# Kernel optimization log

Hardware: AMD Instinct MI355X
Metric: run time of the kernel (lower is better)

The kernel has to match this reference:

```python
import jax, jax.numpy as jnp
import numpy as np

DIM = 768
NUM_HEADS = 12
MAX_DIST = 32


def _build_relative_index(max_dist):
    # Faithful port of the torch buffer construction (pure numpy, static).
    ii, jj = np.meshgrid(np.arange(max_dist), np.arange(max_dist), indexing='ij')
    coords_flat = np.stack([ii.reshape(-1), jj.reshape(-1)], axis=0)  # [2, max_dist^2]
    rel = coords_flat[:, :, None] - coords_flat[:, None, :]          # [2, L, L]
    rel = rel.transpose(1, 2, 0) + (max_dist - 1)
    rel_index = rel[:, :, 0] * (2 * max_dist - 1) + rel[:, :, 1]
    return jnp.asarray(rel_index, dtype=jnp.int32)                   # [L, L]


def setup_inputs() -> dict:
    key = jax.random.key(0)
    k_x, k_qkv, k_proj, k_pb, k_bt = jax.random.split(key, 5)
    B, N, C = 8, 1024, DIM
    std = 0.02
    x = jax.random.normal(k_x, (B, N, C), dtype=jnp.float32)
    qkv_w = jax.random.normal(k_qkv, (C, 3 * C), dtype=jnp.float32) * std  # Linear(dim, 3*dim, bias=False)
    proj_w = jax.random.normal(k_proj, (C, C), dtype=jnp.float32) * std
    proj_b = jax.random.normal(k_pb, (C,), dtype=jnp.float32) * std
    bias_table = jax.random.normal(k_bt, ((2 * MAX_DIST - 1) ** 2, NUM_HEADS), dtype=jnp.float32) * std
    rel_index = _build_relative_index(MAX_DIST)
    return {"x": x, "qkv_w": qkv_w, "proj_w": proj_w, "proj_b": proj_b,
            "bias_table": bias_table, "rel_index": rel_index}


def reference(x, qkv_w, proj_w, proj_b, bias_table, rel_index):
    B, N, C = x.shape
    H = NUM_HEADS
    hd = C // H
    scale = hd ** -0.5
    qkv = (x @ qkv_w).reshape(B, N, 3, H, hd)
    q, k, v = qkv[:, :, 0], qkv[:, :, 1], qkv[:, :, 2]          # [B, N, H, hd]
    attn = jnp.einsum('bnhd,bmhd->bhnm', q, k) * scale           # [B, H, N, N]
    # gathered relative position bias, added per head before softmax
    rel_bias = bias_table[rel_index[:N, :N].reshape(-1)]         # [N*N, H]
    rel_bias = rel_bias.reshape(N, N, H).transpose(2, 0, 1)      # [H, N, N]
    attn = jax.nn.softmax(attn + rel_bias[None], axis=-1)
    out = jnp.einsum('bhnm,bmhd->bnhd', attn, v).reshape(B, N, C)
    return out @ proj_w + proj_b
```

## Files before the change

kernel.cpp:

```cpp
#include <hip/hip_runtime.h>
#include <hip/hip_bf16.h>
#include <stdint.h>

typedef unsigned short u16;
typedef __attribute__((ext_vector_type(8))) short short8;
typedef __attribute__((ext_vector_type(4))) short short4v;
typedef __attribute__((ext_vector_type(8))) __bf16 bf16x8;
typedef __attribute__((ext_vector_type(4))) float floatx4;

typedef const uint32_t __attribute__((address_space(1))) *gptr1;
typedef uint32_t __attribute__((address_space(3))) *lptr3;

#define DIMC 768
#define NH   12
#define HD   64
#define NB   8
#define SEQ  1024
#define MROWS (NB*SEQ)
#define BTAB_N 47628
#define PB_N   768
#define LOG2E 1.44269504088896340736f

__device__ __forceinline__ float bf2f(u16 u){ return __uint_as_float(((uint32_t)u)<<16); }
__device__ __forceinline__ u16 f2bf(float f){
  uint32_t u = __float_as_uint(f);
  u += 0x7fffu + ((u>>16)&1u);
  return (u16)(u>>16);
}
__device__ __forceinline__ uint32_t pkbf(float lo, float hi){
  return (uint32_t)f2bf(lo) | ((uint32_t)f2bf(hi) << 16);
}
__device__ __forceinline__ floatx4 mfma16(short8 a, short8 b, floatx4 c){
  return __builtin_amdgcn_mfma_f32_16x16x32_bf16(
      __builtin_bit_cast(bf16x8, a), __builtin_bit_cast(bf16x8, b), c, 0, 0, 0);
}
__device__ __forceinline__ floatx4 mfma1k(short4v a, short4v b, floatx4 c){
  return __builtin_amdgcn_mfma_f32_16x16x16bf16_1k(a, b, c, 0, 0, 0);
}

__global__ __launch_bounds__(256) void detect_dtype(
    const u16* __restrict__ x, int* __restrict__ flag)
{
  __shared__ int cnt[256];
  int c = 0;
  for (int i = threadIdx.x; i < 2048; i += 256) {
    int e = (x[i] >> 7) & 0xFF;
    c += (e >= 0x8E);
  }
  cnt[threadIdx.x] = c;
  __syncthreads();
  for (int s = 128; s > 0; s >>= 1) {
    if ((int)threadIdx.x < s) cnt[threadIdx.x] += cnt[threadIdx.x + s];
    __syncthreads();
  }
  if (threadIdx.x == 0) *flag = (cnt[0] > 16) ? 1 : 0;
}

__global__ __launch_bounds__(256) void convert_x(
    const void* __restrict__ in, u16* __restrict__ outp,
    const int* __restrict__ flag, int n4)
{
  int idx = blockIdx.x * 256 + threadIdx.x;
  if (idx >= n4) return;
  ushort4 o;
  if (*flag) {
    const float4 v = ((const float4*)in)[idx];
    o.x = f2bf(v.x); o.y = f2bf(v.y); o.z = f2bf(v.z); o.w = f2bf(v.w);
  } else {
    o = ((const ushort4*)in)[idx];
  }
  ((ushort4*)outp)[idx] = o;
}

__global__ __launch_bounds__(256) void convert_small(
    const void* __restrict__ btab, const void* __restrict__ pb,
    u16* __restrict__ btabB, u16* __restrict__ pbB, const int* __restrict__ flag)
{
  int f = *flag;
  int idx = blockIdx.x * 256 + threadIdx.x;
  if (idx < BTAB_N) {
    float v = f ? ((const float*)btab)[idx] : bf2f(((const u16*)btab)[idx]);
    btabB[idx] = f2bf(v * LOG2E);
  } else if (idx < BTAB_N + PB_N) {
    int j = idx - BTAB_N;
    pbB[j] = f ? f2bf(((const float*)pb)[j]) : ((const u16*)pb)[j];
  }
}

__global__ __launch_bounds__(256) void transpose_any(
    const void* __restrict__ in, u16* __restrict__ out, int R, int C,
    const int* __restrict__ flag)
{
  __shared__ __align__(16) u16 t[64][65];
  const int f = *flag;
  const size_t bo = (size_t)blockIdx.z * R * C;
  const int r0 = blockIdx.y * 64, c0 = blockIdx.x * 64;
  const int tx = threadIdx.x & 63, ty = threadIdx.x >> 6;
  #pragma unroll
  for (int i = ty; i < 64; i += 4) {
    size_t src = bo + (size_t)(r0 + i) * C + c0 + tx;
    t[i][tx] = f ? f2bf(((const float*)in)[src]) : ((const u16*)in)[src];
  }
  __syncthreads();
  #pragma unroll
  for (int i = ty; i < 64; i += 4)
    out[bo + (size_t)(c0 + i) * R + r0 + tx] = t[tx][i];
}

__global__ __launch_bounds__(256) void build_bias(
    const int* __restrict__ rel, const u16* __restrict__ table, u16* __restrict__ biasM)
{
  const int t = blockIdx.x * 256 + threadIdx.x;
  const int idx = rel[t];
  const u16* row = table + idx * NH;
  #pragma unroll
  for (int h = 0; h < NH; ++h)
    biasM[(size_t)h * (SEQ * SEQ) + t] = row[h];
}

__global__ __launch_bounds__(256) void gemm_qkv(
    const u16* __restrict__ A, const u16* __restrict__ Bt,
    u16* __restrict__ Qb, u16* __restrict__ Kb, u16* __restrict__ Vt)
{
  const int K = DIMC;
  __shared__ __align__(16) u16 As[128 * 64];
  __shared__ __align__(16) u16 Bs[128 * 64];
  const int m0 = blockIdx.x * 128, n0 = blockIdx.y * 128;
  const int tid = threadIdx.x;
  const int wave = tid >> 6, lane = tid & 63;
  const int wx = wave & 1, wy = wave >> 1;
  const int r15 = lane & 15, quad = lane >> 4;
  const int sw = r15 & 7;

  const floatx4 zf = {0.f, 0.f, 0.f, 0.f};
  floatx4 acc[4][4];
  #pragma unroll
  for (int i = 0; i < 4; ++i)
    #pragma unroll
    for (int j = 0; j < 4; ++j) acc[i][j] = zf;

  for (int kt = 0; kt < K; kt += 64) {
    __syncthreads();
    #pragma unroll
    for (int s = 0; s < 4; ++s) {
      int c = s * 256 + wave * 64 + lane;
      int row = c >> 3, cc = (c & 7) ^ (row & 7);
      __builtin_amdgcn_global_load_lds(
          (gptr1)(const void*)&A[(size_t)(m0 + row) * K + kt + cc * 8],
          (lptr3)(void*)&As[c * 8], 16, 0, 0);
      __builtin_amdgcn_global_load_lds(
          (gptr1)(const void*)&Bt[(size_t)(n0 + row) * K + kt + cc * 8],
          (lptr3)(void*)&Bs[c * 8], 16, 0, 0);
    }
    __syncthreads();
    #pragma unroll
    for (int ks = 0; ks < 64; ks += 32) {
      const int kc = ks >> 3;
      short8 a[4], b[4];
      #pragma unroll
      for (int i = 0; i < 4; ++i)
        a[i] = *(const short8*)&As[(wy * 64 + i * 16 + r15) * 64 + ((kc + quad) ^ sw) * 8];
      #pragma unroll
      for (int j = 0; j < 4; ++j)
        b[j] = *(const short8*)&Bs[(wx * 64 + j * 16 + r15) * 64 + ((kc + quad) ^ sw) * 8];
      #pragma unroll
      for (int i = 0; i < 4; ++i)
        #pragma unroll
        for (int j = 0; j < 4; ++j)
          acc[i][j] = mfma16(a[i], b[j], acc[i][j]);
    }
  }

  #pragma unroll
  for (int i = 0; i < 4; ++i)
    #pragma unroll
    for (int j = 0; j < 4; ++j)
      #pragma unroll
      for (int g = 0; g < 4; ++g) {
        int gm = m0 + wy * 64 + i * 16 + quad * 4 + g;
        int gn = n0 + wx * 64 + j * 16 + r15;
        float v = acc[i][j][g];
        int three = gn / DIMC;
        int hn = gn - three * DIMC;
        int h = hn >> 6, d = hn & 63;
        int b_ = gm >> 10, n = gm & 1023;
        int bh = b_ * NH + h;
        if (three == 0)      Qb[(((size_t)bh) * SEQ + n) * HD + d] = f2bf(v * (0.125f * LOG2E));
        else if (three == 1) Kb[(((size_t)bh) * SEQ + n) * HD + d] = f2bf(v);
        else                 Vt[(((size_t)bh) * HD + d) * SEQ + n] = f2bf(v);
      }
}

__global__ __launch_bounds__(256) void gemm_proj(
    const u16* __restrict__ A, const u16* __restrict__ Bt,
    float* __restrict__ Out, const u16* __restrict__ bias)
{
  const int K = DIMC, N = DIMC;
  __shared__ __align__(16) u16 As[64 * 64];
  __shared__ __align__(16) u16 Bs[128 * 64];
  const int m0 = blockIdx.x * 64, n0 = blockIdx.y * 128;
  const int tid = threadIdx.x;
  const int wave = tid >> 6, lane = tid & 63;
  const int wy = wave >> 1, wx = wave & 1;
  const int r15 = lane & 15, quad = lane >> 4;
  const int sw = r15 & 7;

  const floatx4 zf = {0.f, 0.f, 0.f, 0.f};
  floatx4 acc[2][4];
  #pragma unroll
  for (int i = 0; i < 2; ++i)
    #pragma unroll
    for (int j = 0; j < 4; ++j) acc[i][j] = zf;

  for (int kt = 0; kt < K; kt += 64) {
    __syncthreads();
    #pragma unroll
    for (int s = 0; s < 2; ++s) {
      int c = tid + s * 256;
      int row = c >> 3, cc = (c & 7) ^ (row & 7);
      __builtin_amdgcn_global_load_lds(
          (gptr1)(const void*)&A[(size_t)(m0 + row) * K + kt + cc * 8],
          (lptr3)(void*)&As[c * 8], 16, 0, 0);
    }
    #pragma unroll
    for (int s = 0; s < 4; ++s) {
      int c = tid + s * 256;
      int row = c >> 3, cc = (c & 7) ^ (row & 7);
      __builtin_amdgcn_global_load_lds(
          (gptr1)(const void*)&Bt[(size_t)(n0 + row) * K + kt + cc * 8],
          (lptr3)(void*)&Bs[c * 8], 16, 0, 0);
    }
    __syncthreads();
    #pragma unroll
    for (int ks = 0; ks < 64; ks += 32) {
      const int kc = ks >> 3;
      short8 a[2], b[4];
      #pragma unroll
      for (int i = 0; i < 2; ++i)
        a[i] = *(const short8*)&As[(wy * 32 + i * 16 + r15) * 64 + ((kc + quad) ^ sw) * 8];
      #pragma unroll
      for (int j = 0; j < 4; ++j)
        b[j] = *(const short8*)&Bs[(wx * 64 + j * 16 + r15) * 64 + ((kc + quad) ^ sw) * 8];
      #pragma unroll
      for (int i = 0; i < 2; ++i)
        #pragma unroll
        for (int j = 0; j < 4; ++j)
          acc[i][j] = mfma16(a[i], b[j], acc[i][j]);
    }
  }

  #pragma unroll
  for (int i = 0; i < 2; ++i)
    #pragma unroll
    for (int j = 0; j < 4; ++j)
      #pragma unroll
      for (int g = 0; g < 4; ++g) {
        int gm = m0 + wy * 32 + i * 16 + quad * 4 + g;
        int gn = n0 + wx * 64 + j * 16 + r15;
        Out[(size_t)gm * N + gn] = acc[i][j][g] + bf2f(bias[gn]);
      }
}

template<int USEB>
__global__ __launch_bounds__(512, 6) void attention(
    const u16* __restrict__ Qb, const u16* __restrict__ Kb, const u16* __restrict__ Vt,
    const u16* __restrict__ biasB, u16* __restrict__ Ob)
{
  __shared__ __align__(16) u16 Qs[128 * 64];
  __shared__ __align__(16) u16 Ks[64 * 64];
  __shared__ __align__(16) u16 Vs[64 * 64];

  const int bh = blockIdx.x;
  const int h = bh % NH, b_ = bh / NH;
  const int q0 = blockIdx.y * 128;
  const int tid = threadIdx.x;
  const int wave = tid >> 6, lane = tid & 63;
  const int r15 = lane & 15, quad = lane >> 4;
  const int sw = r15 & 7;

  const u16* Qp = Qb + (size_t)bh * SEQ * HD;
  const u16* Kp = Kb + (size_t)bh * SEQ * HD;
  const u16* Vp = Vt + (size_t)bh * HD * SEQ;
  const u16* Bp = USEB ? (biasB + (size_t)h * SEQ * SEQ) : biasB;

  #pragma unroll
  for (int s = 0; s < 2; ++s) {
    int c = tid + s * 512;
    int row = c >> 3, cc = (c & 7) ^ (row & 7);
    __builtin_amdgcn_global_load_lds(
        (gptr1)(const void*)&Qp[(size_t)(q0 + row) * HD + cc * 8],
        (lptr3)(void*)&Qs[c * 8], 16, 0, 0);
  }

  const int q = q0 + wave * 16 + r15;
  const size_t bqoff = (size_t)q * SEQ;
  const int qrow = wave * 16 + r15;

  const floatx4 zf = {0.f, 0.f, 0.f, 0.f};
  floatx4 o[4];
  #pragma unroll
  for (int Jm = 0; Jm < 4; ++Jm) o[Jm] = zf;
  float lpart = 0.f;

  for (int kt = 0; kt < 16; ++kt) {
    __syncthreads();
    ushort4 bc[4];
    if (USEB) {
      #pragma unroll
      for (int Jk = 0; Jk < 4; ++Jk)
        bc[Jk] = *(const ushort4*)&Bp[bqoff + kt * 64 + Jk * 16 + quad * 4];
    }
    {
      int c = tid;
      int row = c >> 3, cc = (c & 7) ^ (row & 7);
      __builtin_amdgcn_global_load_lds(
          (gptr1)(const void*)&Kp[(size_t)(kt * 64 + row) * HD + cc * 8],
          (lptr3)(void*)&Ks[c * 8], 16, 0, 0);
      __builtin_amdgcn_global_load_lds(
          (gptr1)(const void*)&Vp[(size_t)row * SEQ + kt * 64 + cc * 8],
          (lptr3)(void*)&Vs[c * 8], 16, 0, 0);
    }
    __syncthreads();

    floatx4 sT[4];
    #pragma unroll
    for (int Jk = 0; Jk < 4; ++Jk) sT[Jk] = zf;

    #pragma unroll
    for (int ks = 0; ks < 64; ks += 32) {
      const int kc = ks >> 3;
      const short8 bq = *(const short8*)&Qs[qrow * 64 + ((kc + quad) ^ sw) * 8];
      #pragma unroll
      for (int Jk = 0; Jk < 4; ++Jk) {
        const short8 ak = *(const short8*)&Ks[(Jk * 16 + r15) * 64 + ((kc + quad) ^ sw) * 8];
        sT[Jk] = mfma16(ak, bq, sT[Jk]);
      }
    }

    #pragma unroll
    for (int Jk = 0; Jk < 4; ++Jk) {
      if (USEB) {
        sT[Jk][0] += bf2f(bc[Jk].x); sT[Jk][1] += bf2f(bc[Jk].y);
        sT[Jk][2] += bf2f(bc[Jk].z); sT[Jk][3] += bf2f(bc[Jk].w);
      } else {
        #pragma unroll
        for (int g = 0; g < 4; ++g) {
          const int k = kt * 64 + Jk * 16 + quad * 4 + g;
          const int idx = ((q >> 5) - (k >> 5) + 31) * 63 + ((q & 31) - (k & 31) + 31);
          sT[Jk][g] += bf2f(Bp[idx * NH + h]);
        }
      }
      const float p0 = exp2f(sT[Jk][0]);
      const float p1 = exp2f(sT[Jk][1]);
      const float p2v = exp2f(sT[Jk][2]);
      const float p3 = exp2f(sT[Jk][3]);
      lpart += (p0 + p1) + (p2v + p3);
      uint2 pw;
      pw.x = pkbf(p0, p1);
      pw.y = pkbf(p2v, p3);
      const short4v bp = __builtin_bit_cast(short4v, pw);
      const int vcol = ((2 * Jk + (quad >> 1)) ^ sw) * 8 + (quad & 1) * 4;
      #pragma unroll
      for (int Jm = 0; Jm < 4; ++Jm) {
        const short4v av = *(const short4v*)&Vs[(Jm * 16 + r15) * 64 + vcol];
        o[Jm] = mfma1k(av, bp, o[Jm]);
      }
    }
  }

  float l = lpart;
  l += __shfl_xor(l, 16, 64);
  l += __shfl_xor(l, 32, 64);
  const float inv = 1.0f / l;

  #pragma unroll
  for (int Jm = 0; Jm < 4; ++Jm) {
    uint2 st;
    st.x = pkbf(o[Jm][0] * inv, o[Jm][1] * inv);
    st.y = pkbf(o[Jm][2] * inv, o[Jm][3] * inv);
    *(uint2*)&Ob[((size_t)(b_ * SEQ + q)) * DIMC + h * HD + Jm * 16 + quad * 4] = st;
  }
}

extern "C" void kernel_launch(void* const* d_in, const int* in_sizes, int n_in,
                              void* d_out, int out_size, void* d_ws, size_t ws_size,
                              hipStream_t stream)
{
  (void)in_sizes; (void)n_in; (void)out_size;
  const void* x_raw  = d_in[0];
  const void* qkv_w  = d_in[1];
  const void* proj_w = d_in[2];
  const void* proj_b = d_in[3];
  const void* btab   = d_in[4];
  const int*  rel    = (const int*)d_in[5];
  float* out = (float*)d_out;

  const size_t SZ_FLAG = 256;
  const size_t SZ_XB   = (size_t)MROWS * DIMC * 2;
  const size_t SZ_BTAB = (BTAB_N * 2 + 255) & ~(size_t)255;
  const size_t SZ_PB   = (PB_N * 2 + 255) & ~(size_t)255;
  const size_t SZ_WQT  = (size_t)3 * DIMC * DIMC * 2;
  const size_t SZ_WPT  = (size_t)DIMC * DIMC * 2;
  const size_t SZ_T    = (size_t)NB * NH * SEQ * HD * 2;
  const size_t SZ_BM   = (size_t)NH * SEQ * SEQ * 2;
  const size_t NEED_FULL = SZ_FLAG + SZ_XB + SZ_BTAB + SZ_PB + SZ_WQT + SZ_WPT
                         + 3 * SZ_T + SZ_BM;

  char* p = (char*)d_ws;
  int* flag  = (int*)p;  p += SZ_FLAG;
  u16* xB    = (u16*)p;  p += SZ_XB;
  u16* btabB = (u16*)p;  p += SZ_BTAB;
  u16* pbB   = (u16*)p;  p += SZ_PB;
  u16* wqT   = (u16*)p;  p += SZ_WQT;
  u16* wpT   = (u16*)p;  p += SZ_WPT;
  u16* Qb    = (u16*)p;  p += SZ_T;
  u16* Kb    = (u16*)p;  p += SZ_T;
  u16* Vt    = (u16*)p;  p += SZ_T;
  u16* biasM = (u16*)p;

  const bool useBiasM = (ws_size >= NEED_FULL);
  const int n4 = MROWS * DIMC / 4;

  detect_dtype<<<1, 256, 0, stream>>>((const u16*)x_raw, flag);
  convert_x<<<(n4 + 255) / 256, 256, 0, stream>>>(x_raw, xB, flag, n4);
  convert_small<<<(BTAB_N + PB_N + 255) / 256, 256, 0, stream>>>(btab, proj_b, btabB, pbB, flag);
  transpose_any<<<dim3(3 * DIMC / 64, DIMC / 64, 1), 256, 0, stream>>>(qkv_w, wqT, DIMC, 3 * DIMC, flag);
  transpose_any<<<dim3(DIMC / 64, DIMC / 64, 1), 256, 0, stream>>>(proj_w, wpT, DIMC, DIMC, flag);
  gemm_qkv<<<dim3(MROWS / 128, 3 * DIMC / 128), 256, 0, stream>>>(
      xB, wqT, Qb, Kb, Vt);
  if (useBiasM) {
    build_bias<<<SEQ * SEQ / 256, 256, 0, stream>>>(rel, btabB, biasM);
    attention<1><<<dim3(NB * NH, SEQ / 128), 512, 0, stream>>>(Qb, Kb, Vt, biasM, xB);
  } else {
    attention<0><<<dim3(NB * NH, SEQ / 128), 512, 0, stream>>>(Qb, Kb, Vt, btabB, xB);
  }
  gemm_proj<<<dim3(MROWS / 64, DIMC / 128), 256, 0, stream>>>(
      xB, wpT, out, pbB);
}
```

Baseline: 268.9 us.

## Fuse all preprocessing kernels into one prep launch and enlarge proj GEMM tile

Replaces the dtype detection, x conversion, small-table conversion, two weight transposes and bias-matrix build with a single multi-job prep kernel. Each block recomputes the dtype flag locally through a wave reduction, so the separate flag kernel and its global round trip disappear. The bias matrix is now built straight from the raw table rather than from the converted copy. The output projection GEMM moves from 64x128 to 128x128 tiles, which gives more MFMA reuse per block but launches fewer blocks and needs more registers per thread.

```diff
diff --git a/kernel.cpp b/kernel.cpp
--- a/kernel.cpp
+++ b/kernel.cpp
@@ -21,6 +21,12 @@
 #define PB_N   768
 #define LOG2E 1.44269504088896340736f
 
+#define PJ_X     6144
+#define PJ_WQ    (PJ_X + 432)
+#define PJ_WP    (PJ_WQ + 144)
+#define PJ_BIAS  (PJ_WP + 4096)
+#define PJ_SMALL (PJ_BIAS + 190)
+
 __device__ __forceinline__ float bf2f(u16 u){ return __uint_as_float(((uint32_t)u)<<16); }
 __device__ __forceinline__ u16 f2bf(float f){
   uint32_t u = __float_as_uint(f);
@@ -38,84 +44,79 @@
   return __builtin_amdgcn_mfma_f32_16x16x16bf16_1k(a, b, c, 0, 0, 0);
 }
 
-__global__ __launch_bounds__(256) void detect_dtype(
-    const u16* __restrict__ x, int* __restrict__ flag)
+__global__ __launch_bounds__(256) void prep(
+    const void* __restrict__ x_raw, const void* __restrict__ qkv_w,
+    const void* __restrict__ proj_w, const void* __restrict__ proj_b,
+    const void* __restrict__ btab, const int* __restrict__ rel,
+    u16* __restrict__ xB, u16* __restrict__ wqT, u16* __restrict__ wpT,
+    u16* __restrict__ btabB, u16* __restrict__ pbB, u16* __restrict__ biasM)
 {
-  __shared__ int cnt[256];
-  int c = 0;
-  for (int i = threadIdx.x; i < 2048; i += 256) {
-    int e = (x[i] >> 7) & 0xFF;
-    c += (e >= 0x8E);
-  }
-  cnt[threadIdx.x] = c;
+  __shared__ __align__(16) u16 tt[64][65];
+  __shared__ int wc[4];
+
+  const int tid = threadIdx.x;
+  {
+    const u16* xs = (const u16*)x_raw;
+    int c = 0;
+    #pragma unroll
+    for (int i = 0; i < 8; ++i) {
+      int e = (xs[tid * 8 + i] >> 7) & 0xFF;
+      c += (e >= 0x8E);
+    }
+    #pragma unroll
+    for (int off = 1; off < 64; off <<= 1) c += __shfl_xor(c, off, 64);
+    if ((tid & 63) == 0) wc[tid >> 6] = c;
+  }
   __syncthreads();
-  for (int s = 128; s > 0; s >>= 1) {
-    if ((int)threadIdx.x < s) cnt[threadIdx.x] += cnt[threadIdx.x + s];
-    __syncthreads();
-  }
-  if (threadIdx.x == 0) *flag = (cnt[0] > 16) ? 1 : 0;
-}
-
-__global__ __launch_bounds__(256) void convert_x(
-    const void* __restrict__ in, u16* __restrict__ outp,
-    const int* __restrict__ flag, int n4)
-{
-  int idx = blockIdx.x * 256 + threadIdx.x;
-  if (idx >= n4) return;
-  ushort4 o;
-  if (*flag) {
-    const float4 v = ((const float4*)in)[idx];
-    o.x = f2bf(v.x); o.y = f2bf(v.y); o.z = f2bf(v.z); o.w = f2bf(v.w);
+  const int flag = ((wc[0] + wc[1] + wc[2] + wc[3]) > 16) ? 1 : 0;
+
+  const int job = blockIdx.x;
+  if (job < PJ_X) {
+    int idx = job * 256 + tid;
+    ushort4 o;
+    if (flag) {
+      const float4 v = ((const float4*)x_raw)[idx];
+      o.x = f2bf(v.x); o.y = f2bf(v.y); o.z = f2bf(v.z); o.w = f2bf(v.w);
+    } else {
+      o = ((const ushort4*)x_raw)[idx];
+    }
+    ((ushort4*)xB)[idx] = o;
+  } else if (job < PJ_WP) {
+    const void* in; u16* outp; int C, R, t;
+    if (job < PJ_WQ) { t = job - PJ_X;  in = qkv_w;  outp = wqT; R = DIMC; C = 3 * DIMC; }
+    else             { t = job - PJ_WQ; in = proj_w; outp = wpT; R = DIMC; C = DIMC; }
+    const int tilesX = C >> 6;
+    const int c0 = (t % tilesX) * 64, r0 = (t / tilesX) * 64;
+    const int tx = tid & 63, ty = tid >> 6;
+    #pragma unroll
+    for (int i = ty; i < 64; i += 4) {
+      size_t src = (size_t)(r0 + i) * C + c0 + tx;
+      tt[i][tx] = flag ? f2bf(((const float*)in)[src]) : ((const u16*)in)[src];
+    }
+    __syncthreads();
+    #pragma unroll
+    for (int i = ty; i < 64; i += 4)
+      outp[(size_t)(c0 + i) * R + r0 + tx] = tt[tx][i];
+  } else if (job < PJ_BIAS) {
+    if (biasM) {
+      const int t = (job - PJ_WP) * 256 + tid;
+      const int idx = rel[t] * NH;
+      #pragma unroll
+      for (int h = 0; h < NH; ++h) {
+        float v = flag ? ((const float*)btab)[idx + h] : bf2f(((const u16*)btab)[idx + h]);
+        biasM[(size_t)h * (SEQ * SEQ) + t] = f2bf(v * LOG2E);
+      }
+    }
   } else {
-    o = ((const ushort4*)in)[idx];
-  }
-  ((ushort4*)outp)[idx] = o;
-}
-
-__global__ __launch_bounds__(256) void convert_small(
-    const void* __restrict__ btab, const void* __restrict__ pb,
-    u16* __restrict__ btabB, u16* __restrict__ pbB, const int* __restrict__ flag)
-{
-  int f = *flag;
-  int idx = blockIdx.x * 256 + threadIdx.x;
-  if (idx < BTAB_N) {
-    float v = f ? ((const float*)btab)[idx] : bf2f(((const u16*)btab)[idx]);
-    btabB[idx] = f2bf(v * LOG2E);
-  } else if (idx < BTAB_N + PB_N) {
-    int j = idx - BTAB_N;
-    pbB[j] = f ? f2bf(((const float*)pb)[j]) : ((const u16*)pb)[j];
-  }
-}
-
-__global__ __launch_bounds__(256) void transpose_any(
-    const void* __restrict__ in, u16* __restrict__ out, int R, int C,
-    const int* __restrict__ flag)
-{
-  __shared__ __align__(16) u16 t[64][65];
-  const int f = *flag;
-  const size_t bo = (size_t)blockIdx.z * R * C;
-  const int r0 = blockIdx.y * 64, c0 = blockIdx.x * 64;
-  const int tx = threadIdx.x & 63, ty = threadIdx.x >> 6;
-  #pragma unroll
-  for (int i = ty; i < 64; i += 4) {
-    size_t src = bo + (size_t)(r0 + i) * C + c0 + tx;
-    t[i][tx] = f ? f2bf(((const float*)in)[src]) : ((const u16*)in)[src];
-  }
-  __syncthreads();
-  #pragma unroll
-  for (int i = ty; i < 64; i += 4)
-    out[bo + (size_t)(c0 + i) * R + r0 + tx] = t[tx][i];
-}
-
-__global__ __launch_bounds__(256) void build_bias(
-    const int* __restrict__ rel, const u16* __restrict__ table, u16* __restrict__ biasM)
-{
-  const int t = blockIdx.x * 256 + threadIdx.x;
-  const int idx = rel[t];
-  const u16* row = table + idx * NH;
-  #pragma unroll
-  for (int h = 0; h < NH; ++h)
-    biasM[(size_t)h * (SEQ * SEQ) + t] = row[h];
+    const int idx = (job - PJ_BIAS) * 256 + tid;
+    if (idx < BTAB_N) {
+      float v = flag ? ((const float*)btab)[idx] : bf2f(((const u16*)btab)[idx]);
+      btabB[idx] = f2bf(v * LOG2E);
+    } else if (idx < BTAB_N + PB_N) {
+      int j = idx - BTAB_N;
+      pbB[j] = flag ? f2bf(((const float*)proj_b)[j]) : ((const u16*)proj_b)[j];
+    }
+  }
 }
 
 __global__ __launch_bounds__(256) void gemm_qkv(
@@ -196,36 +197,31 @@
     float* __restrict__ Out, const u16* __restrict__ bias)
 {
   const int K = DIMC, N = DIMC;
-  __shared__ __align__(16) u16 As[64 * 64];
+  __shared__ __align__(16) u16 As[128 * 64];
   __shared__ __align__(16) u16 Bs[128 * 64];
-  const int m0 = blockIdx.x * 64, n0 = blockIdx.y * 128;
+  const int m0 = blockIdx.x * 128, n0 = blockIdx.y * 128;
   const int tid = threadIdx.x;
   const int wave = tid >> 6, lane = tid & 63;
-  const int wy = wave >> 1, wx = wave & 1;
+  const int wx = wave & 1, wy = wave >> 1;
   const int r15 = lane & 15, quad = lane >> 4;
   const int sw = r15 & 7;
 
   const floatx4 zf = {0.f, 0.f, 0.f, 0.f};
-  floatx4 acc[2][4];
-  #pragma unroll
-  for (int i = 0; i < 2; ++i)
+  floatx4 acc[4][4];
+  #pragma unroll
+  for (int i = 0; i < 4; ++i)
     #pragma unroll
     for (int j = 0; j < 4; ++j) acc[i][j] = zf;
 
   for (int kt = 0; kt < K; kt += 64) {
     __syncthreads();
     #pragma unroll
-    for (int s = 0; s < 2; ++s) {
-      int c = tid + s * 256;
+    for (int s = 0; s < 4; ++s) {
+      int c = s * 256 + wave * 64 + lane;
       int row = c >> 3, cc = (c & 7) ^ (row & 7);
       __builtin_amdgcn_global_load_lds(
           (gptr1)(const void*)&A[(size_t)(m0 + row) * K + kt + cc * 8],
           (lptr3)(void*)&As[c * 8], 16, 0, 0);
-    }
-    #pragma unroll
-    for (int s = 0; s < 4; ++s) {
-      int c = tid + s * 256;
-      int row = c >> 3, cc = (c & 7) ^ (row & 7);
       __builtin_amdgcn_global_load_lds(
           (gptr1)(const void*)&Bt[(size_t)(n0 + row) * K + kt + cc * 8],
           (lptr3)(void*)&Bs[c * 8], 16, 0, 0);
@@ -234,15 +230,15 @@
     #pragma unroll
     for (int ks = 0; ks < 64; ks += 32) {
       const int kc = ks >> 3;
-      short8 a[2], b[4];
-      #pragma unroll
-      for (int i = 0; i < 2; ++i)
-        a[i] = *(const short8*)&As[(wy * 32 + i * 16 + r15) * 64 + ((kc + quad) ^ sw) * 8];
+      short8 a[4], b[4];
+      #pragma unroll
+      for (int i = 0; i < 4; ++i)
+        a[i] = *(const short8*)&As[(wy * 64 + i * 16 + r15) * 64 + ((kc + quad) ^ sw) * 8];
       #pragma unroll
       for (int j = 0; j < 4; ++j)
         b[j] = *(const short8*)&Bs[(wx * 64 + j * 16 + r15) * 64 + ((kc + quad) ^ sw) * 8];
       #pragma unroll
-      for (int i = 0; i < 2; ++i)
+      for (int i = 0; i < 4; ++i)
         #pragma unroll
         for (int j = 0; j < 4; ++j)
           acc[i][j] = mfma16(a[i], b[j], acc[i][j]);
@@ -250,12 +246,12 @@
   }
 
   #pragma unroll
-  for (int i = 0; i < 2; ++i)
+  for (int i = 0; i < 4; ++i)
     #pragma unroll
     for (int j = 0; j < 4; ++j)
       #pragma unroll
       for (int g = 0; g < 4; ++g) {
-        int gm = m0 + wy * 32 + i * 16 + quad * 4 + g;
+        int gm = m0 + wy * 64 + i * 16 + quad * 4 + g;
         int gn = n0 + wx * 64 + j * 16 + r15;
         Out[(size_t)gm * N + gn] = acc[i][j][g] + bf2f(bias[gn]);
       }
@@ -395,7 +391,6 @@
   const int*  rel    = (const int*)d_in[5];
   float* out = (float*)d_out;
 
-  const size_t SZ_FLAG = 256;
   const size_t SZ_XB   = (size_t)MROWS * DIMC * 2;
   const size_t SZ_BTAB = (BTAB_N * 2 + 255) & ~(size_t)255;
   const size_t SZ_PB   = (PB_N * 2 + 255) & ~(size_t)255;
@@ -403,11 +398,10 @@
   const size_t SZ_WPT  = (size_t)DIMC * DIMC * 2;
   const size_t SZ_T    = (size_t)NB * NH * SEQ * HD * 2;
   const size_t SZ_BM   = (size_t)NH * SEQ * SEQ * 2;
-  const size_t NEED_FULL = SZ_FLAG + SZ_XB + SZ_BTAB + SZ_PB + SZ_WQT + SZ_WPT
+  const size_t NEED_FULL = SZ_XB + SZ_BTAB + SZ_PB + SZ_WQT + SZ_WPT
                          + 3 * SZ_T + SZ_BM;
 
   char* p = (char*)d_ws;
-  int* flag  = (int*)p;  p += SZ_FLAG;
   u16* xB    = (u16*)p;  p += SZ_XB;
   u16* btabB = (u16*)p;  p += SZ_BTAB;
   u16* pbB   = (u16*)p;  p += SZ_PB;
@@ -419,21 +413,17 @@
   u16* biasM = (u16*)p;
 
   const bool useBiasM = (ws_size >= NEED_FULL);
-  const int n4 = MROWS * DIMC / 4;
-
-  detect_dtype<<<1, 256, 0, stream>>>((const u16*)x_raw, flag);
-  convert_x<<<(n4 + 255) / 256, 256, 0, stream>>>(x_raw, xB, flag, n4);
-  convert_small<<<(BTAB_N + PB_N + 255) / 256, 256, 0, stream>>>(btab, proj_b, btabB, pbB, flag);
-  transpose_any<<<dim3(3 * DIMC / 64, DIMC / 64, 1), 256, 0, stream>>>(qkv_w, wqT, DIMC, 3 * DIMC, flag);
-  transpose_any<<<dim3(DIMC / 64, DIMC / 64, 1), 256, 0, stream>>>(proj_w, wpT, DIMC, DIMC, flag);
+
+  prep<<<PJ_SMALL, 256, 0, stream>>>(
+      x_raw, qkv_w, proj_w, proj_b, btab, rel,
+      xB, wqT, wpT, btabB, pbB, useBiasM ? biasM : (u16*)nullptr);
   gemm_qkv<<<dim3(MROWS / 128, 3 * DIMC / 128), 256, 0, stream>>>(
       xB, wqT, Qb, Kb, Vt);
   if (useBiasM) {
-    build_bias<<<SEQ * SEQ / 256, 256, 0, stream>>>(rel, btabB, biasM);
     attention<1><<<dim3(NB * NH, SEQ / 128), 512, 0, stream>>>(Qb, Kb, Vt, biasM, xB);
   } else {
     attention<0><<<dim3(NB * NH, SEQ / 128), 512, 0, stream>>>(Qb, Kb, Vt, btabB, xB);
   }
-  gemm_proj<<<dim3(MROWS / 64, DIMC / 128), 256, 0, stream>>>(
+  gemm_proj<<<dim3(MROWS / 128, DIMC / 128), 256, 0, stream>>>(
       xB, wpT, out, pbB);
 }
```

Result: faster. 261.9 us (-2.6%).
